# Kernel optimization log

Hardware: AMD Instinct MI355X
Metric: run time of the kernel (lower is better)

The kernel has to match this reference:

```python
import jax, jax.numpy as jnp
import numpy as np

N, M, E, C_IN, C_OUT = 100000, 20000, 1600000, 128, 128


def _safe_inv(d):
    # 1/d with 0 where d==0 (matches PyG D[D==inf]=0), grad-safe
    safe = jnp.where(d > 0, d, 1.0)
    return jnp.where(d > 0, 1.0 / safe, 0.0)


def _hconv(x, node_idx, edge_idx, hw, W, b):
    # PyG HypergraphConv, use_attention=False, heads=1:
    # X' = D^{-1} H B^{-1} H^T (X Theta) + bias, D uses hyperedge_weight
    xt = x @ W  # [N, C_OUT]
    D = jax.ops.segment_sum(hw[edge_idx], node_idx, num_segments=N)
    Dinv = _safe_inv(D)  # [N]
    Bc = jax.ops.segment_sum(jnp.ones((E,), dtype=x.dtype), edge_idx, num_segments=M)
    Binv = _safe_inv(Bc)  # [M]
    # node -> hyperedge (message weighted by B^{-1} of target edge)
    e = jax.ops.segment_sum(Binv[edge_idx][:, None] * xt[node_idx], edge_idx, num_segments=M)
    # hyperedge -> node (message weighted by D^{-1} of target node)
    out = jax.ops.segment_sum(Dinv[node_idx][:, None] * e[edge_idx], node_idx, num_segments=N)
    return out + b


def setup_inputs() -> dict:
    key = jax.random.key(0)
    ks = jax.random.split(key, 12)
    x = jax.random.normal(ks[0], (N, C_IN), dtype=jnp.float32)
    node_idx = jax.random.randint(ks[1], (E,), 0, N, dtype=jnp.int32)
    edge_idx = jax.random.randint(ks[2], (E,), 0, M, dtype=jnp.int32)
    hyperedge_index = jnp.stack([node_idx, edge_idx])
    hyperedge_weight = jax.random.uniform(ks[3], (M,), dtype=jnp.float32) + 0.5
    hyperedge_attr = jax.random.normal(ks[4], (M, C_IN), dtype=jnp.float32)
    batch = jnp.zeros((N,), dtype=jnp.int32)
    s1 = 1.0 / np.sqrt(C_IN)
    s2 = 1.0 / np.sqrt(C_OUT)
    W1 = jax.random.uniform(ks[5], (C_IN, C_OUT), minval=-s1, maxval=s1, dtype=jnp.float32)
    W2 = jax.random.uniform(ks[6], (C_OUT, C_OUT), minval=-s2, maxval=s2, dtype=jnp.float32)
    W3 = jax.random.uniform(ks[7], (C_OUT, C_OUT), minval=-s2, maxval=s2, dtype=jnp.float32)
    b1 = jax.random.uniform(ks[8], (C_OUT,), minval=-s1, maxval=s1, dtype=jnp.float32)
    b2 = jax.random.uniform(ks[9], (C_OUT,), minval=-s2, maxval=s2, dtype=jnp.float32)
    b3 = jax.random.uniform(ks[10], (C_OUT,), minval=-s2, maxval=s2, dtype=jnp.float32)
    return {"x": x, "hyperedge_index": hyperedge_index, "hyperedge_weight": hyperedge_weight,
            "hyperedge_attr": hyperedge_attr, "batch": batch,
            "W1": W1, "b1": b1, "W2": W2, "b2": b2, "W3": W3, "b3": b3}


def reference(x, hyperedge_index, hyperedge_weight, hyperedge_attr, batch,
              W1, b1, W2, b2, W3, b3):
    node_idx = hyperedge_index[0]
    edge_idx = hyperedge_index[1]
    # dropout is identity in eval mode; hyperedge_attr/batch unused (no attention)
    h = jax.nn.relu(_hconv(x, node_idx, edge_idx, hyperedge_weight, W1, b1))
    h = jax.nn.relu(_hconv(h, node_idx, edge_idx, hyperedge_weight, W2, b2))
    h = jax.nn.relu(_hconv(h, node_idx, edge_idx, hyperedge_weight, W3, b3))
    return h
```

## Files before the change

### kernel.cpp

```cpp
#include <hip/hip_runtime.h>
#include <hip/hip_fp16.h>

#define NN 100000
#define MM 20000
#define EE 1600000

#define SCAN_BLOCK 256
#define SCAN_ITEMS 8
#define SCAN_TILE (SCAN_BLOCK * SCAN_ITEMS)
#define NB_E ((MM + SCAN_TILE - 1) / SCAN_TILE)
#define NB_N ((NN + SCAN_TILE - 1) / SCAN_TILE)
#define NB_TOT (NB_E + NB_N)

static inline size_t align256(size_t x) { return (x + 255) & ~(size_t)255; }

struct alignas(8) half4 { __half2 lo, hi; };

__device__ __forceinline__ float4 h4_to_f4(half4 v) {
  float2 a = __half22float2(v.lo);
  float2 b = __half22float2(v.hi);
  return make_float4(a.x, a.y, b.x, b.y);
}
__device__ __forceinline__ half4 f4_to_h4(float4 v) {
  half4 r;
  r.lo = __float22half2_rn(make_float2(v.x, v.y));
  r.hi = __float22half2_rn(make_float2(v.z, v.w));
  return r;
}

__global__ void zero_i32_kernel(int* __restrict__ p, int n) {
  int i = blockIdx.x * blockDim.x + threadIdx.x;
  int stride = gridDim.x * blockDim.x;
  for (; i < n; i += stride) p[i] = 0;
}

__global__ __launch_bounds__(256) void cvt_f2h_kernel(
    const float* __restrict__ in, __half* __restrict__ out, int n4) {
  int i = blockIdx.x * 256 + threadIdx.x;
  int stride = gridDim.x * 256;
  for (; i < n4; i += stride) {
    float4 v = ((const float4*)in)[i];
    ((half4*)out)[i] = f4_to_h4(v);
  }
}

__global__ __launch_bounds__(256) void count_kernel(
    const int* __restrict__ node_idx, const int* __restrict__ edge_idx,
    int* __restrict__ ecnt, int* __restrict__ ncnt,
    unsigned int* __restrict__ rank_packed) {
  int i = blockIdx.x * 256 + threadIdx.x;
  if (i >= EE / 4) return;
  int4 nv = ((const int4*)node_idx)[i];
  int4 ev = ((const int4*)edge_idx)[i];
  int n[4] = {nv.x, nv.y, nv.z, nv.w};
  int e[4] = {ev.x, ev.y, ev.z, ev.w};
  unsigned int rp[4];
#pragma unroll
  for (int j = 0; j < 4; ++j) {
    unsigned int p = (unsigned int)atomicAdd(&ecnt[e[j]], 1);
    unsigned int q = (unsigned int)atomicAdd(&ncnt[n[j]], 1);
    rp[j] = (p & 0xFFFFu) | (q << 16);
  }
  ((uint4*)rank_packed)[i] = make_uint4(rp[0], rp[1], rp[2], rp[3]);
}

__global__ __launch_bounds__(SCAN_BLOCK) void scan_partial_kernel(
    const int* __restrict__ ecnt, const int* __restrict__ ncnt,
    int* __restrict__ eptr, int* __restrict__ nptr, int* __restrict__ bsum) {
  __shared__ int lds[SCAN_BLOCK];
  int b = blockIdx.x;
  const int* cnt; int* ptr; int len; int lb;
  if (b < NB_E) { cnt = ecnt; ptr = eptr; len = MM; lb = b; }
  else          { cnt = ncnt; ptr = nptr; len = NN; lb = b - NB_E; }
  int t = threadIdx.x;
  int lo = lb * SCAN_TILE + t * SCAN_ITEMS;
  int v[SCAN_ITEMS];
  int s = 0;
#pragma unroll
  for (int j = 0; j < SCAN_ITEMS; ++j) {
    int idx = lo + j;
    v[j] = (idx < len) ? cnt[idx] : 0;
    s += v[j];
  }
  lds[t] = s;
  __syncthreads();
  for (int d = 1; d < SCAN_BLOCK; d <<= 1) {
    int o = (t >= d) ? lds[t - d] : 0;
    __syncthreads();
    lds[t] += o;
    __syncthreads();
  }
  int run = lds[t] - s;
#pragma unroll
  for (int j = 0; j < SCAN_ITEMS; ++j) {
    int idx = lo + j;
    if (idx < len) ptr[idx] = run;
    run += v[j];
  }
  if (t == SCAN_BLOCK - 1) bsum[b] = lds[t];
}

__global__ void scan_bsum_kernel(int* __restrict__ bsum) {
  int t = threadIdx.x;
  if (t == 0) {
    int run = 0;
    for (int i = 0; i < NB_E; ++i) { int c = bsum[i]; bsum[i] = run; run += c; }
  } else if (t == 1) {
    int run = 0;
    for (int i = NB_E; i < NB_TOT; ++i) { int c = bsum[i]; bsum[i] = run; run += c; }
  }
}

__global__ __launch_bounds__(SCAN_BLOCK) void scan_fixup_kernel(
    int* __restrict__ eptr, int* __restrict__ nptr,
    const int* __restrict__ ecnt, const int* __restrict__ bsum,
    float* __restrict__ Binv) {
  int b = blockIdx.x;
  int* ptr; int len; int lb; bool isE;
  if (b < NB_E) { ptr = eptr; len = MM; lb = b; isE = true; }
  else          { ptr = nptr; len = NN; lb = b - NB_E; isE = false; }
  int boff = bsum[b];
  int t = threadIdx.x;
  int lo = lb * SCAN_TILE + t * SCAN_ITEMS;
#pragma unroll
  for (int j = 0; j < SCAN_ITEMS; ++j) {
    int idx = lo + j;
    if (idx < len) {
      ptr[idx] += boff;
      if (isE) {
        int c = ecnt[idx];
        Binv[idx] = (c > 0) ? 1.0f / (float)c : 0.0f;
      }
    }
  }
  if (b == 0 && t == 0) { eptr[MM] = EE; nptr[NN] = EE; }
}

__global__ __launch_bounds__(256) void fill_kernel(
    const int* __restrict__ node_idx, const int* __restrict__ edge_idx,
    const int* __restrict__ eptr, const int* __restrict__ nptr,
    const unsigned int* __restrict__ rank_packed,
    int* __restrict__ edge_nodes, int* __restrict__ node_edges) {
  int i = blockIdx.x * 256 + threadIdx.x;
  if (i >= EE / 4) return;
  int4 nv = ((const int4*)node_idx)[i];
  int4 ev = ((const int4*)edge_idx)[i];
  uint4 rv = ((const uint4*)rank_packed)[i];
  int n[4] = {nv.x, nv.y, nv.z, nv.w};
  int e[4] = {ev.x, ev.y, ev.z, ev.w};
  unsigned int rp[4] = {rv.x, rv.y, rv.z, rv.w};
#pragma unroll
  for (int j = 0; j < 4; ++j) {
    edge_nodes[eptr[e[j]] + (int)(rp[j] & 0xFFFFu)] = n[j];
    node_edges[nptr[n[j]] + (int)(rp[j] >> 16)] = e[j];
  }
}

__global__ __launch_bounds__(256) void dinv_csr_kernel(
    const int* __restrict__ nptr, const int* __restrict__ node_edges,
    const float* __restrict__ hw, float* __restrict__ Dinv) {
  int n = blockIdx.x * 256 + threadIdx.x;
  if (n >= NN) return;
  int lo = nptr[n], hi = nptr[n + 1];
  float d = 0.0f;
  for (int j = lo; j < hi; ++j) d += hw[node_edges[j]];
  Dinv[n] = (d > 0.0f) ? 1.0f / d : 0.0f;
}

__device__ __forceinline__ void fma4(float4& acc, float s, const float4& m) {
  acc.x += s * m.x;
  acc.y += s * m.y;
  acc.z += s * m.z;
  acc.w += s * m.w;
}

__global__ __launch_bounds__(256) void gemm128_kernel(
    const __half* __restrict__ X, const float* __restrict__ W,
    __half* __restrict__ Y, int nrows) {
  __shared__ float Wl[128 * 128];
  float4* Wl4 = (float4*)Wl;
  const float4* W4 = (const float4*)W;
  for (int i = threadIdx.x; i < 128 * 32; i += 256) Wl4[i] = W4[i];
  __syncthreads();

  int tc = threadIdx.x & 15;
  int tr = threadIdx.x >> 4;
  int base = blockIdx.x * 64;
  int r[4];
  bool v[4];
#pragma unroll
  for (int j = 0; j < 4; ++j) {
    int rr = base + tr + j * 16;
    v[j] = rr < nrows;
    r[j] = v[j] ? rr : 0;
  }
  float4 acc[4][2];
#pragma unroll
  for (int j = 0; j < 4; ++j) {
    acc[j][0] = make_float4(0.f, 0.f, 0.f, 0.f);
    acc[j][1] = make_float4(0.f, 0.f, 0.f, 0.f);
  }
#pragma unroll 4
  for (int k4 = 0; k4 < 32; ++k4) {
    float4 xv[4];
#pragma unroll
    for (int j = 0; j < 4; ++j)
      xv[j] = h4_to_f4(((const half4*)X)[(size_t)r[j] * 32 + k4]);
#pragma unroll
    for (int kk = 0; kk < 4; ++kk) {
      float4 wva = Wl4[(k4 * 4 + kk) * 32 + tc];
      float4 wvb = Wl4[(k4 * 4 + kk) * 32 + 16 + tc];
#pragma unroll
      for (int j = 0; j < 4; ++j) {
        float xk = ((const float*)&xv[j])[kk];
        fma4(acc[j][0], xk, wva);
        fma4(acc[j][1], xk, wvb);
      }
    }
  }
#pragma unroll
  for (int j = 0; j < 4; ++j) {
    if (v[j]) {
      ((half4*)Y)[(size_t)r[j] * 32 + tc] = f4_to_h4(acc[j][0]);
      ((half4*)Y)[(size_t)r[j] * 32 + 16 + tc] = f4_to_h4(acc[j][1]);
    }
  }
}

__global__ __launch_bounds__(256) void edge_agg_kernel(
    const __half* __restrict__ hin, const int* __restrict__ eptr,
    const int* __restrict__ edge_nodes, const float* __restrict__ Binv,
    __half* __restrict__ eout) {
  int half_id = threadIdx.x >> 5;
  int lane = threadIdx.x & 31;
  int m = blockIdx.x * 8 + half_id;
  if (m >= MM) return;
  int lo = eptr[m], hi = eptr[m + 1];
  const half4* h4p = (const half4*)hin;
  float4 acc = make_float4(0.f, 0.f, 0.f, 0.f);
  int j = lo;
  for (; j + 4 <= hi; j += 4) {
    int n0 = edge_nodes[j + 0];
    int n1 = edge_nodes[j + 1];
    int n2 = edge_nodes[j + 2];
    int n3 = edge_nodes[j + 3];
    float4 a = h4_to_f4(h4p[(size_t)n0 * 32 + lane]);
    float4 b = h4_to_f4(h4p[(size_t)n1 * 32 + lane]);
    float4 c = h4_to_f4(h4p[(size_t)n2 * 32 + lane]);
    float4 d = h4_to_f4(h4p[(size_t)n3 * 32 + lane]);
    acc.x += (a.x + b.x) + (c.x + d.x);
    acc.y += (a.y + b.y) + (c.y + d.y);
    acc.z += (a.z + b.z) + (c.z + d.z);
    acc.w += (a.w + b.w) + (c.w + d.w);
  }
  for (; j < hi; ++j) {
    int n = edge_nodes[j];
    float4 a = h4_to_f4(h4p[(size_t)n * 32 + lane]);
    acc.x += a.x; acc.y += a.y; acc.z += a.z; acc.w += a.w;
  }
  float bi = Binv[m];
  acc.x *= bi; acc.y *= bi; acc.z *= bi; acc.w *= bi;
  ((half4*)eout)[(size_t)m * 32 + lane] = f4_to_h4(acc);
}

__device__ __forceinline__ void strow(float* Y, size_t i, float4 v) {
  ((float4*)Y)[i] = v;
}
__device__ __forceinline__ void strow(__half* Y, size_t i, float4 v) {
  ((half4*)Y)[i] = f4_to_h4(v);
}

template <typename TOUT>
__global__ __launch_bounds__(256) void node_agg_kernel(
    const __half* __restrict__ ein, const int* __restrict__ nptr,
    const int* __restrict__ node_edges, const float* __restrict__ Dinv,
    const float* __restrict__ bias, TOUT* __restrict__ out) {
  int half_id = threadIdx.x >> 5;
  int lane = threadIdx.x & 31;
  int n = blockIdx.x * 8 + half_id;
  if (n >= NN) return;
  int lo = nptr[n], hi = nptr[n + 1];
  const half4* e4 = (const half4*)ein;
  float4 acc = make_float4(0.f, 0.f, 0.f, 0.f);
  int j = lo;
  for (; j + 4 <= hi; j += 4) {
    int m0 = node_edges[j + 0];
    int m1 = node_edges[j + 1];
    int m2 = node_edges[j + 2];
    int m3 = node_edges[j + 3];
    float4 a = h4_to_f4(e4[(size_t)m0 * 32 + lane]);
    float4 b = h4_to_f4(e4[(size_t)m1 * 32 + lane]);
    float4 c = h4_to_f4(e4[(size_t)m2 * 32 + lane]);
    float4 d = h4_to_f4(e4[(size_t)m3 * 32 + lane]);
    acc.x += (a.x + b.x) + (c.x + d.x);
    acc.y += (a.y + b.y) + (c.y + d.y);
    acc.z += (a.z + b.z) + (c.z + d.z);
    acc.w += (a.w + b.w) + (c.w + d.w);
  }
  for (; j < hi; ++j) {
    int m = node_edges[j];
    float4 a = h4_to_f4(e4[(size_t)m * 32 + lane]);
    acc.x += a.x; acc.y += a.y; acc.z += a.z; acc.w += a.w;
  }
  float di = Dinv[n];
  float4 bb = ((const float4*)bias)[lane];
  float4 rv;
  rv.x = fmaxf(di * acc.x + bb.x, 0.f);
  rv.y = fmaxf(di * acc.y + bb.y, 0.f);
  rv.z = fmaxf(di * acc.z + bb.z, 0.f);
  rv.w = fmaxf(di * acc.w + bb.w, 0.f);
  strow(out, (size_t)n * 32 + lane, rv);
}

extern "C" void kernel_launch(void* const* d_in, const int* in_sizes, int n_in,
                              void* d_out, int out_size, void* d_ws, size_t ws_size,
                              hipStream_t stream) {
  const float* x = (const float*)d_in[0];
  const int* hidx = (const int*)d_in[1];
  const int* node_idx = hidx;
  const int* edge_idx = hidx + EE;
  const float* hw = (const float*)d_in[2];
  const float* W1 = (const float*)d_in[5];
  const float* b1 = (const float*)d_in[6];
  const float* W2 = (const float*)d_in[7];
  const float* b2 = (const float*)d_in[8];
  const float* W3 = (const float*)d_in[9];
  const float* b3 = (const float*)d_in[10];
  float* out = (float*)d_out;

  char* ws = (char*)d_ws;
  size_t off = 0;
  auto alloc = [&](size_t bytes) -> char* {
    char* p = ws + off;
    off = align256(off + bytes);
    return p;
  };
  __half* xh   = (__half*)alloc(sizeof(__half) * (size_t)NN * 128);
  __half* h    = (__half*)alloc(sizeof(__half) * (size_t)NN * 128);
  __half* eraw = (__half*)alloc(sizeof(__half) * (size_t)MM * 128);
  __half* et   = (__half*)alloc(sizeof(__half) * (size_t)MM * 128);
  int*   zr    = (int*)alloc(sizeof(int) * (size_t)(MM + NN));
  int*   ecnt  = zr;
  int*   ncnt  = zr + MM;
  int*   eptr  = (int*)alloc(sizeof(int) * (MM + 1));
  int*   nptr  = (int*)alloc(sizeof(int) * (NN + 1));
  int*   bsum  = (int*)alloc(sizeof(int) * NB_TOT);
  float* Binv  = (float*)alloc(sizeof(float) * MM);
  float* Dinv  = (float*)alloc(sizeof(float) * NN);
  unsigned int* rank_packed = (unsigned int*)alloc(sizeof(int) * (size_t)EE);
  int* edge_nodes = (int*)alloc(sizeof(int) * (size_t)EE);
  int* node_edges = (int*)alloc(sizeof(int) * (size_t)EE);
  (void)ws_size; (void)in_sizes; (void)n_in; (void)out_size;

  const int quad_grid = (EE / 4 + 255) / 256;

  zero_i32_kernel<<<256, 256, 0, stream>>>(zr, MM + NN);
  count_kernel<<<quad_grid, 256, 0, stream>>>(node_idx, edge_idx, ecnt, ncnt,
                                              rank_packed);
  scan_partial_kernel<<<NB_TOT, SCAN_BLOCK, 0, stream>>>(ecnt, ncnt, eptr, nptr, bsum);
  scan_bsum_kernel<<<1, 64, 0, stream>>>(bsum);
  scan_fixup_kernel<<<NB_TOT, SCAN_BLOCK, 0, stream>>>(eptr, nptr, ecnt, bsum, Binv);
  fill_kernel<<<quad_grid, 256, 0, stream>>>(node_idx, edge_idx, eptr, nptr,
                                             rank_packed, edge_nodes, node_edges);
  dinv_csr_kernel<<<(NN + 255) / 256, 256, 0, stream>>>(nptr, node_edges, hw, Dinv);
  cvt_f2h_kernel<<<1024, 256, 0, stream>>>(x, xh, NN * 32);

  const int gemmE_grid = (MM + 63) / 64;
  const int eagg_grid = MM / 8;
  const int nagg_grid = NN / 8;

  edge_agg_kernel<<<eagg_grid, 256, 0, stream>>>(xh, eptr, edge_nodes, Binv, eraw);
  gemm128_kernel<<<gemmE_grid, 256, 0, stream>>>(eraw, W1, et, MM);
  node_agg_kernel<__half><<<nagg_grid, 256, 0, stream>>>(et, nptr, node_edges,
                                                         Dinv, b1, h);
  edge_agg_kernel<<<eagg_grid, 256, 0, stream>>>(h, eptr, edge_nodes, Binv, eraw);
  gemm128_kernel<<<gemmE_grid, 256, 0, stream>>>(eraw, W2, et, MM);
  node_agg_kernel<__half><<<nagg_grid, 256, 0, stream>>>(et, nptr, node_edges,
                                                         Dinv, b2, xh);
  edge_agg_kernel<<<eagg_grid, 256, 0, stream>>>(xh, eptr, edge_nodes, Binv, eraw);
  gemm128_kernel<<<gemmE_grid, 256, 0, stream>>>(eraw, W3, et, MM);
  node_agg_kernel<float><<<nagg_grid, 256, 0, stream>>>(et, nptr, node_edges,
                                                        Dinv, b3, out);
}
```

Baseline: 629.4 us.

## Replace global atomic CSR counting with per-block LDS histograms and column scans

Builds the edge and node CSR structures by having each block histogram a contiguous chunk of incidences in shared memory, recording local ranks, and writing per-block count rows. Column scans over these rows give per-block offsets, and the fill kernel computes slots from the row pointer, block offset and local rank. This removes contended global atomics and the zeroing kernel, but adds large per-block count matrices that must be written, scanned and gathered.

Result: no change. 628.9 us (-0.1%).

```diff
diff --git a/kernel.cpp b/kernel.cpp
--- a/kernel.cpp
+++ b/kernel.cpp
@@ -4,6 +4,12 @@
 #define NN 100000
 #define MM 20000
 #define EE 1600000
+
+#define NBLK_E 256
+#define CHUNK_E (EE / NBLK_E)
+#define NBLK_N 128
+#define CHUNK_N (EE / NBLK_N)
+#define NRANGE 25000
 
 #define SCAN_BLOCK 256
 #define SCAN_ITEMS 8
@@ -26,12 +32,6 @@
   r.lo = __float22half2_rn(make_float2(v.x, v.y));
   r.hi = __float22half2_rn(make_float2(v.z, v.w));
   return r;
-}
-
-__global__ void zero_i32_kernel(int* __restrict__ p, int n) {
-  int i = blockIdx.x * blockDim.x + threadIdx.x;
-  int stride = gridDim.x * blockDim.x;
-  for (; i < n; i += stride) p[i] = 0;
 }
 
 __global__ __launch_bounds__(256) void cvt_f2h_kernel(
@@ -44,24 +44,76 @@
   }
 }
 
-__global__ __launch_bounds__(256) void count_kernel(
-    const int* __restrict__ node_idx, const int* __restrict__ edge_idx,
-    int* __restrict__ ecnt, int* __restrict__ ncnt,
-    unsigned int* __restrict__ rank_packed) {
-  int i = blockIdx.x * 256 + threadIdx.x;
-  if (i >= EE / 4) return;
-  int4 nv = ((const int4*)node_idx)[i];
-  int4 ev = ((const int4*)edge_idx)[i];
-  int n[4] = {nv.x, nv.y, nv.z, nv.w};
-  int e[4] = {ev.x, ev.y, ev.z, ev.w};
-  unsigned int rp[4];
-#pragma unroll
-  for (int j = 0; j < 4; ++j) {
-    unsigned int p = (unsigned int)atomicAdd(&ecnt[e[j]], 1);
-    unsigned int q = (unsigned int)atomicAdd(&ncnt[n[j]], 1);
-    rp[j] = (p & 0xFFFFu) | (q << 16);
-  }
-  ((uint4*)rank_packed)[i] = make_uint4(rp[0], rp[1], rp[2], rp[3]);
+__global__ __launch_bounds__(256) void ehist_kernel(
+    const int* __restrict__ edge_idx,
+    int* __restrict__ bcnt_e, unsigned short* __restrict__ lrank_e) {
+  extern __shared__ int hist[];
+  int b = blockIdx.x;
+  for (int k = threadIdx.x; k < MM; k += 256) hist[k] = 0;
+  __syncthreads();
+  int lo = b * CHUNK_E, hi = lo + CHUNK_E;
+  for (int i = lo + threadIdx.x; i < hi; i += 256) {
+    int e = edge_idx[i];
+    int r = atomicAdd(&hist[e], 1);
+    lrank_e[i] = (unsigned short)r;
+  }
+  __syncthreads();
+  int* row = bcnt_e + (size_t)b * MM;
+  for (int k = threadIdx.x; k < MM; k += 256) row[k] = hist[k];
+}
+
+__global__ __launch_bounds__(256) void nhist_kernel(
+    const int* __restrict__ node_idx,
+    int* __restrict__ bcnt_n, unsigned short* __restrict__ lrank_n) {
+  extern __shared__ int hist[];
+  int b = blockIdx.x;
+  int lo = b * CHUNK_N, hi = lo + CHUNK_N;
+  int* row = bcnt_n + (size_t)b * NN;
+  for (int p = 0; p < 4; ++p) {
+    int base = p * NRANGE;
+    for (int k = threadIdx.x; k < NRANGE; k += 256) hist[k] = 0;
+    __syncthreads();
+    for (int i = lo + threadIdx.x; i < hi; i += 256) {
+      int n = node_idx[i] - base;
+      if ((unsigned)n < (unsigned)NRANGE) {
+        int r = atomicAdd(&hist[n], 1);
+        lrank_n[i] = (unsigned short)r;
+      }
+    }
+    __syncthreads();
+    for (int k = threadIdx.x; k < NRANGE; k += 256) row[base + k] = hist[k];
+    __syncthreads();
+  }
+}
+
+__global__ __launch_bounds__(256) void colscan_e_kernel(
+    int* __restrict__ bcnt_e, int* __restrict__ ecnt) {
+  int e = blockIdx.x * 256 + threadIdx.x;
+  if (e >= MM) return;
+  int run = 0;
+#pragma unroll 8
+  for (int b = 0; b < NBLK_E; ++b) {
+    size_t idx = (size_t)b * MM + e;
+    int v = bcnt_e[idx];
+    bcnt_e[idx] = run;
+    run += v;
+  }
+  ecnt[e] = run;
+}
+
+__global__ __launch_bounds__(256) void colscan_n_kernel(
+    int* __restrict__ bcnt_n, int* __restrict__ ncnt) {
+  int n = blockIdx.x * 256 + threadIdx.x;
+  if (n >= NN) return;
+  int run = 0;
+#pragma unroll 8
+  for (int b = 0; b < NBLK_N; ++b) {
+    size_t idx = (size_t)b * NN + n;
+    int v = bcnt_n[idx];
+    bcnt_n[idx] = run;
+    run += v;
+  }
+  ncnt[n] = run;
 }
 
 __global__ __launch_bounds__(SCAN_BLOCK) void scan_partial_kernel(
@@ -136,24 +188,23 @@
   if (b == 0 && t == 0) { eptr[MM] = EE; nptr[NN] = EE; }
 }
 
-__global__ __launch_bounds__(256) void fill_kernel(
+__global__ __launch_bounds__(256) void fill2_kernel(
     const int* __restrict__ node_idx, const int* __restrict__ edge_idx,
     const int* __restrict__ eptr, const int* __restrict__ nptr,
-    const unsigned int* __restrict__ rank_packed,
+    const int* __restrict__ bcnt_e, const int* __restrict__ bcnt_n,
+    const unsigned short* __restrict__ lrank_e,
+    const unsigned short* __restrict__ lrank_n,
     int* __restrict__ edge_nodes, int* __restrict__ node_edges) {
   int i = blockIdx.x * 256 + threadIdx.x;
-  if (i >= EE / 4) return;
-  int4 nv = ((const int4*)node_idx)[i];
-  int4 ev = ((const int4*)edge_idx)[i];
-  uint4 rv = ((const uint4*)rank_packed)[i];
-  int n[4] = {nv.x, nv.y, nv.z, nv.w};
-  int e[4] = {ev.x, ev.y, ev.z, ev.w};
-  unsigned int rp[4] = {rv.x, rv.y, rv.z, rv.w};
-#pragma unroll
-  for (int j = 0; j < 4; ++j) {
-    edge_nodes[eptr[e[j]] + (int)(rp[j] & 0xFFFFu)] = n[j];
-    node_edges[nptr[n[j]] + (int)(rp[j] >> 16)] = e[j];
-  }
+  if (i >= EE) return;
+  int e = edge_idx[i];
+  int n = node_idx[i];
+  int be = i / CHUNK_E;
+  int bn = i / CHUNK_N;
+  int slotE = eptr[e] + bcnt_e[(size_t)be * MM + e] + (int)lrank_e[i];
+  edge_nodes[slotE] = n;
+  int slotN = nptr[n] + bcnt_n[(size_t)bn * NN + n] + (int)lrank_n[i];
+  node_edges[slotN] = e;
 }
 
 __global__ __launch_bounds__(256) void dinv_csr_kernel(
@@ -339,29 +390,31 @@
   __half* h    = (__half*)alloc(sizeof(__half) * (size_t)NN * 128);
   __half* eraw = (__half*)alloc(sizeof(__half) * (size_t)MM * 128);
   __half* et   = (__half*)alloc(sizeof(__half) * (size_t)MM * 128);
-  int*   zr    = (int*)alloc(sizeof(int) * (size_t)(MM + NN));
-  int*   ecnt  = zr;
-  int*   ncnt  = zr + MM;
+  int*   bcnt_e = (int*)alloc(sizeof(int) * (size_t)NBLK_E * MM);
+  int*   bcnt_n = (int*)alloc(sizeof(int) * (size_t)NBLK_N * NN);
+  unsigned short* lrank_e = (unsigned short*)alloc(sizeof(short) * (size_t)EE);
+  unsigned short* lrank_n = (unsigned short*)alloc(sizeof(short) * (size_t)EE);
+  int*   ecnt  = (int*)alloc(sizeof(int) * MM);
+  int*   ncnt  = (int*)alloc(sizeof(int) * NN);
   int*   eptr  = (int*)alloc(sizeof(int) * (MM + 1));
   int*   nptr  = (int*)alloc(sizeof(int) * (NN + 1));
   int*   bsum  = (int*)alloc(sizeof(int) * NB_TOT);
   float* Binv  = (float*)alloc(sizeof(float) * MM);
   float* Dinv  = (float*)alloc(sizeof(float) * NN);
-  unsigned int* rank_packed = (unsigned int*)alloc(sizeof(int) * (size_t)EE);
   int* edge_nodes = (int*)alloc(sizeof(int) * (size_t)EE);
   int* node_edges = (int*)alloc(sizeof(int) * (size_t)EE);
   (void)ws_size; (void)in_sizes; (void)n_in; (void)out_size;
 
-  const int quad_grid = (EE / 4 + 255) / 256;
-
-  zero_i32_kernel<<<256, 256, 0, stream>>>(zr, MM + NN);
-  count_kernel<<<quad_grid, 256, 0, stream>>>(node_idx, edge_idx, ecnt, ncnt,
-                                              rank_packed);
+  ehist_kernel<<<NBLK_E, 256, MM * sizeof(int), stream>>>(edge_idx, bcnt_e, lrank_e);
+  nhist_kernel<<<NBLK_N, 256, NRANGE * sizeof(int), stream>>>(node_idx, bcnt_n, lrank_n);
+  colscan_e_kernel<<<(MM + 255) / 256, 256, 0, stream>>>(bcnt_e, ecnt);
+  colscan_n_kernel<<<(NN + 255) / 256, 256, 0, stream>>>(bcnt_n, ncnt);
   scan_partial_kernel<<<NB_TOT, SCAN_BLOCK, 0, stream>>>(ecnt, ncnt, eptr, nptr, bsum);
   scan_bsum_kernel<<<1, 64, 0, stream>>>(bsum);
   scan_fixup_kernel<<<NB_TOT, SCAN_BLOCK, 0, stream>>>(eptr, nptr, ecnt, bsum, Binv);
-  fill_kernel<<<quad_grid, 256, 0, stream>>>(node_idx, edge_idx, eptr, nptr,
-                                             rank_packed, edge_nodes, node_edges);
+  fill2_kernel<<<(EE + 255) / 256, 256, 0, stream>>>(node_idx, edge_idx, eptr, nptr,
+                                                     bcnt_e, bcnt_n, lrank_e, lrank_n,
+                                                     edge_nodes, node_edges);
   dinv_csr_kernel<<<(NN + 255) / 256, 256, 0, stream>>>(nptr, node_edges, hw, Dinv);
   cvt_f2h_kernel<<<1024, 256, 0, stream>>>(x, xh, NN * 32);
 
```
